# Kernel tuning notes

Hardware: AMD Instinct MI355X
Metric: run time of the kernel (lower is better)

The kernel has to match this reference:

```python
import jax, jax.numpy as jnp
import numpy as np

N, E, G = 50000, 300000, 64
VOCAB, EMB, FEAT = 10000, 64, 8
DIN, DH, EDIM = EMB * FEAT, 256, 6


def _lin(k, fout, fin):
    kw, kb = jax.random.split(k)
    w = jax.random.normal(kw, (fout, fin), jnp.float32) / float(np.sqrt(fin))
    b = jax.random.normal(kb, (fout,), jnp.float32) * 0.01
    return w, b


def setup_inputs() -> dict:
    key = jax.random.key(0)
    ks = jax.random.split(key, 10)
    inp = {
        'x_idx': jax.random.randint(ks[0], (N, FEAT), 0, VOCAB),
        'edge_index': jax.random.randint(ks[1], (2, E), 0, N),
        'edge_attr': jax.random.normal(ks[2], (E, EDIM), jnp.float32),
        'batch': jnp.sort(jax.random.randint(ks[3], (N,), 0, G)),
        'emb_table': jax.random.normal(ks[4], (VOCAB, EMB), jnp.float32) * 0.1,
    }
    # two TransformerConv layers: lin_query/key/value (d_in->DH), lin_edge (EDIM->DH), lin_skip (d_in->DH)
    for li, kbase, din in ((1, ks[5], DIN), (2, ks[6], DH)):
        sub = jax.random.split(kbase, 5)
        for j, (wn, bn, fin) in enumerate([('wq', 'bq', din), ('wk', 'bk', din), ('wv', 'bv', din), ('we', 'be', EDIM), ('ws', 'bs', din)]):
            w, b = _lin(sub[j], DH, fin)
            inp['c%d_%s' % (li, wn)] = w
            inp['c%d_%s' % (li, bn)] = b
    for i, (fout, fin, k) in enumerate([(256, 2 * DH, ks[7]), (128, 256, ks[8]), (1, 128, ks[9])]):
        w, b = _lin(k, fout, fin)
        inp['w%d' % (i + 1)] = w
        inp['b%d' % (i + 1)] = b
    return inp


def _tconv(h, src, dst, edge_attr, wq, bq, wk, bk, wv, bv, we, be, ws, bs):
    # PyG TransformerConv, heads=1, concat=True, root_weight=True, beta=False
    n = h.shape[0]
    q = h @ wq.T + bq                      # [N, DH]
    k = h @ wk.T + bk
    v = h @ wv.T + bv
    e = edge_attr @ we.T + be              # [E, DH]
    ke = k[src] + e                        # key fused with edge features
    logits = jnp.sum(q[dst] * ke, axis=-1) / jnp.sqrt(jnp.float32(DH))  # [E]
    m = jax.ops.segment_max(logits, dst, num_segments=n)
    m = jnp.where(jnp.isfinite(m), m, 0.0)
    a = jnp.exp(logits - m[dst])
    s = jax.ops.segment_sum(a, dst, num_segments=n)
    a = a / s[dst]                         # scatter-softmax over incoming edges
    agg = jax.ops.segment_sum((v[src] + e) * a[:, None], dst, num_segments=n)
    return agg + h @ ws.T + bs             # skip connection (root_weight)


def reference(x_idx, edge_index, edge_attr, batch, emb_table,
              c1_wq, c1_bq, c1_wk, c1_bk, c1_wv, c1_bv, c1_we, c1_be, c1_ws, c1_bs,
              c2_wq, c2_bq, c2_wk, c2_bk, c2_wv, c2_bv, c2_we, c2_be, c2_ws, c2_bs,
              w1, b1, w2, b2, w3, b3):
    x = emb_table[x_idx].reshape(x_idx.shape[0], DIN)  # [N, EMB*FEAT]
    src, dst = edge_index[0], edge_index[1]
    h = jax.nn.relu(_tconv(x, src, dst, edge_attr, c1_wq, c1_bq, c1_wk, c1_bk, c1_wv, c1_bv, c1_we, c1_be, c1_ws, c1_bs))
    h = jax.nn.relu(_tconv(h, src, dst, edge_attr, c2_wq, c2_bq, c2_wk, c2_bk, c2_wv, c2_bv, c2_we, c2_be, c2_ws, c2_bs))
    cnt = jax.ops.segment_sum(jnp.ones((h.shape[0],), h.dtype), batch, num_segments=G)
    gap = jax.ops.segment_sum(h, batch, num_segments=G) / jnp.maximum(cnt, 1.0)[:, None]
    gmp = jax.ops.segment_max(h, batch, num_segments=G)
    gmp = jnp.where(jnp.isfinite(gmp), gmp, 0.0)
    r = jnp.concatenate([gap, gmp], axis=1)             # [G, 2*DH]
    o = jax.nn.relu(r @ w1.T + b1)
    o = jax.nn.relu(o @ w2.T + b2)
    # dropout skipped (eval mode)
    return jax.nn.sigmoid(o @ w3.T + b3)[:, 0]          # [G]
```

## Files before the change

### kernel.cpp

```cpp
#include <hip/hip_runtime.h>

typedef unsigned long long ull;
typedef __bf16 bf16x8 __attribute__((ext_vector_type(8)));
typedef float f32x4 __attribute__((ext_vector_type(4)));

__device__ __forceinline__ float bf2f(unsigned short u) {
  union { unsigned int i; float f; } c; c.i = ((unsigned int)u) << 16; return c.f;
}
__device__ __forceinline__ unsigned short f2bf(float f) {
  union { float f; unsigned int i; } c; c.f = f;
  unsigned int u = c.i;
  u += 0x7fffu + ((u >> 16) & 1u);
  return (unsigned short)(u >> 16);
}

__global__ __launch_bounds__(256) void pack_weights(
    const float* __restrict__ wq, const float* __restrict__ wk,
    const float* __restrict__ wv, const float* __restrict__ ws,
    const float* __restrict__ bq, const float* __restrict__ bk,
    const float* __restrict__ bv, const float* __restrict__ bs,
    unsigned short* __restrict__ Wcat, float* __restrict__ bcat, int logK) {
  int idx = blockIdx.x * 256 + threadIdx.x;
  if (idx < 1024) {
    int rr = idx >> 8, cc = idx & 255;
    const float* bp = (rr == 0) ? bq : (rr == 1) ? bk : (rr == 2) ? bv : bs;
    bcat[idx] = bp[cc];
  }
  int K = 1 << logK;
  if (idx >= (1024 << logK)) return;
  int kj = idx & 7;
  int lane = (idx >> 3) & 63;
  int rg = (idx >> 9) & 3;
  int ksbits = logK - 5;
  int ks = (idx >> 11) & ((1 << ksbits) - 1);
  int colt = idx >> (11 + ksbits);
  int quad = lane >> 4, lm = lane & 15;
  int o = colt * 64 + rg * 16 + lm;
  int k = ks * 32 + quad * 8 + kj;
  int rr = o >> 8, oo = o & 255;
  const float* wp = (rr == 0) ? wq : (rr == 1) ? wk : (rr == 2) ? wv : ws;
  Wcat[idx] = f2bf(wp[oo * K + k]);
}

__global__ __launch_bounds__(256) void embed_gather(
    const int* __restrict__ x_idx, const float* __restrict__ emb,
    unsigned short* __restrict__ xbf, int total) {
  int idx = blockIdx.x * 256 + threadIdx.x;
  if (idx >= total) return;
  int n = idx >> 9, d = idx & 511, f = d >> 6, j = d & 63;
  int vi = x_idx[n * 8 + f];
  int n32 = n >> 5, lm = n & 15, half = (n >> 4) & 1;
  int ks = d >> 5, quad = (d >> 3) & 3, kj = d & 7;
  size_t a = (((size_t)(n32 * 16 + ks)) * 2 + half) * 512 + (quad * 16 + lm) * 8 + kj;
  xbf[a] = f2bf(emb[vi * 64 + j]);
}

__global__ __launch_bounds__(256) void count_dst(const int* __restrict__ dst,
                                                 int* __restrict__ counts, int E_) {
  int i = blockIdx.x * 256 + threadIdx.x;
  if (i < E_) atomicAdd(&counts[dst[i]], 1);
}

__global__ __launch_bounds__(256) void alloc_rows(const int* __restrict__ counts,
                                                  int* __restrict__ row_start,
                                                  int* __restrict__ cursor,
                                                  int* __restrict__ total, int n) {
  int i = blockIdx.x * 256 + threadIdx.x;
  int lane = threadIdx.x & 63;
  int c = (i < n) ? counts[i] : 0;
  int incl = c;
#pragma unroll
  for (int off = 1; off < 64; off <<= 1) {
    int t = __shfl_up(incl, off, 64);
    if (lane >= off) incl += t;
  }
  int base = 0;
  if (lane == 63) base = atomicAdd(total, incl);
  base = __shfl(base, 63, 64);
  int st = base + incl - c;
  if (i < n) { row_start[i] = st; cursor[i] = st; }
}

__global__ __launch_bounds__(256) void scatter_edges(
    const int* __restrict__ dst, const int* __restrict__ srcA,
    const float* __restrict__ eattr, int* __restrict__ cursor,
    int* __restrict__ srcs, float* __restrict__ ea_perm, int E_) {
  int i = blockIdx.x * 256 + threadIdx.x;
  if (i >= E_) return;
  int d = dst[i];
  int p = atomicAdd(&cursor[d], 1);
  srcs[p] = srcA[i];
  const float* ea = eattr + (size_t)i * 6;
  float* eo = ea_perm + (size_t)p * 6;
  eo[0] = ea[0]; eo[1] = ea[1]; eo[2] = ea[2];
  eo[3] = ea[3]; eo[4] = ea[4]; eo[5] = ea[5];
}

template <int K>
__global__ __launch_bounds__(256) void gemm_qkvs(
    const unsigned short* __restrict__ X, const unsigned short* __restrict__ W,
    const float* __restrict__ bcat,
    unsigned short* __restrict__ qout, unsigned short* __restrict__ kout,
    unsigned short* __restrict__ vout, float* __restrict__ sout,
    int Nn, int nrb) {
  __shared__ unsigned short Bs[2][4096];
  const int l = blockIdx.x;
  const int xcd = l & 7, j = l >> 3;
  const int q = nrb >> 3, r = nrb & 7;
  const int cnt = q + (xcd < r ? 1 : 0);
  const int lrb = j >> 4, colt = j & 15;
  if (lrb >= cnt) return;
  const int m_blk = xcd * q + min(xcd, r) + lrb;

  const int tid = threadIdx.x;
  const int wid = tid >> 6;
  const int lane = tid & 63;
  const int quad = lane >> 4, lm = lane & 15;
  const int m_base = m_blk * 128 + wid * 32;
  const int n_base = colt * 64;
  const size_t abase = (size_t)(m_blk * 4 + wid) * (K >> 5) * 1024 + lane * 8;
  const unsigned short* wchunk = W + (size_t)colt * (K >> 5) * 2048;
  const int nc = (K >> 5) >> 1;
  f32x4 acc[2][4] = {};

  {
    bf16x8 st0 = *(const bf16x8*)(wchunk + 0 * 2048 + tid * 8);
    bf16x8 st1 = *(const bf16x8*)(wchunk + 1 * 2048 + tid * 8);
    *(bf16x8*)(&Bs[0][0 * 2048 + tid * 8]) = st0;
    *(bf16x8*)(&Bs[0][1 * 2048 + tid * 8]) = st1;
  }
  __syncthreads();

  for (int c = 0; c < nc; c++) {
    bf16x8 st0, st1;
    const bool pf = (c + 1 < nc);
    if (pf) {
      const unsigned short* wp = wchunk + (size_t)(c + 1) * 4096;
      st0 = *(const bf16x8*)(wp + 0 * 2048 + tid * 8);
      st1 = *(const bf16x8*)(wp + 1 * 2048 + tid * 8);
    }
    const unsigned short* bs = &Bs[c & 1][0];
#pragma unroll
    for (int s = 0; s < 2; s++) {
      const int ks = c * 2 + s;
      const unsigned short* ap = X + abase + (size_t)ks * 1024;
      const unsigned short* bp = bs + s * 2048 + lane * 8;
      bf16x8 a0 = *(const bf16x8*)(ap);
      bf16x8 a1 = *(const bf16x8*)(ap + 512);
      bf16x8 b0 = *(const bf16x8*)(bp);
      bf16x8 b1 = *(const bf16x8*)(bp + 512);
      bf16x8 b2 = *(const bf16x8*)(bp + 1024);
      bf16x8 b3 = *(const bf16x8*)(bp + 1536);
      acc[0][0] = __builtin_amdgcn_mfma_f32_16x16x32_bf16(a0, b0, acc[0][0], 0, 0, 0);
      acc[0][1] = __builtin_amdgcn_mfma_f32_16x16x32_bf16(a0, b1, acc[0][1], 0, 0, 0);
      acc[0][2] = __builtin_amdgcn_mfma_f32_16x16x32_bf16(a0, b2, acc[0][2], 0, 0, 0);
      acc[0][3] = __builtin_amdgcn_mfma_f32_16x16x32_bf16(a0, b3, acc[0][3], 0, 0, 0);
      acc[1][0] = __builtin_amdgcn_mfma_f32_16x16x32_bf16(a1, b0, acc[1][0], 0, 0, 0);
      acc[1][1] = __builtin_amdgcn_mfma_f32_16x16x32_bf16(a1, b1, acc[1][1], 0, 0, 0);
      acc[1][2] = __builtin_amdgcn_mfma_f32_16x16x32_bf16(a1, b2, acc[1][2], 0, 0, 0);
      acc[1][3] = __builtin_amdgcn_mfma_f32_16x16x32_bf16(a1, b3, acc[1][3], 0, 0, 0);
    }
    if (pf) {
      unsigned short* bw = &Bs[(c + 1) & 1][0];
      *(bf16x8*)(bw + 0 * 2048 + tid * 8) = st0;
      *(bf16x8*)(bw + 1 * 2048 + tid * 8) = st1;
    }
    __syncthreads();
  }
#pragma unroll
  for (int mi = 0; mi < 2; mi++) {
#pragma unroll
    for (int r2 = 0; r2 < 4; r2++) {
      int row = m_base + mi * 16 + quad * 4 + r2;
      if (row >= Nn) continue;
      size_t rb = (size_t)row * 256;
#pragma unroll
      for (int ni = 0; ni < 4; ni++) {
        int col = n_base + ni * 16 + lm;
        float v = acc[mi][ni][r2] + bcat[col];
        int reg = col >> 8, c2 = col & 255;
        if (reg == 0)       qout[rb + c2] = f2bf(v * 0.0625f);
        else if (reg == 1)  kout[rb + c2] = f2bf(v);
        else if (reg == 2)  vout[rb + c2] = f2bf(v);
        else                sout[rb + c2] = v;
      }
    }
  }
}

__device__ __forceinline__ float dot4(ull uq, ull uk) {
  return bf2f((unsigned short)uq) * bf2f((unsigned short)uk)
       + bf2f((unsigned short)(uq >> 16)) * bf2f((unsigned short)(uk >> 16))
       + bf2f((unsigned short)(uq >> 32)) * bf2f((unsigned short)(uk >> 32))
       + bf2f((unsigned short)(uq >> 48)) * bf2f((unsigned short)(uk >> 48));
}

#define SEL8_F(a, t) ((t)==0?(a)[0]:(t)==1?(a)[1]:(t)==2?(a)[2]:(t)==3?(a)[3]:(t)==4?(a)[4]:(t)==5?(a)[5]:(t)==6?(a)[6]:(a)[7])

#define NPW 8
__global__ __launch_bounds__(256) void tconv_fused(
    const int* __restrict__ srcs, const int* __restrict__ row_start,
    const int* __restrict__ counts,
    const unsigned short* __restrict__ qv, const unsigned short* __restrict__ kv,
    const unsigned short* __restrict__ vv, const float* __restrict__ ea_perm,
    const float* __restrict__ skipv,
    const float* __restrict__ we, const float* __restrict__ be,
    int Nn, int mode,
    unsigned short* __restrict__ hout, float* __restrict__ h_acc) {
  __shared__ float we_s[1536];
  __shared__ float be_s[256];
  __shared__ float lgt[4][128];
  for (int i = threadIdx.x; i < 1536; i += 256) we_s[i] = we[i];
  be_s[threadIdx.x] = be[threadIdx.x];
  __syncthreads();
  int wid = threadIdx.x >> 6;
  int lane = threadIdx.x & 63;
  int wave = blockIdx.x * 4 + wid;
  int n0 = wave * NPW;
  if (n0 >= Nn) return;
  int n1 = min(n0 + NPW, Nn);
  int j0 = lane * 4;
  float* mylgt = lgt[wid];
  for (int n = n0; n < n1; n++) {
    int cnt = counts[n];
    float a0 = 0.f, a1 = 0.f, a2 = 0.f, a3 = 0.f;
    float e[4] = {0.f, 0.f, 0.f, 0.f};
    if (cnt > 0) {
      int beg = row_start[n];
      ull uqr = *(const ull*)(qv + (size_t)n * 256 + j0);
      float q0 = bf2f((unsigned short)uqr), q1 = bf2f((unsigned short)(uqr >> 16));
      float q2 = bf2f((unsigned short)(uqr >> 32)), q3 = bf2f((unsigned short)(uqr >> 48));
      float z[7];
#pragma unroll
      for (int t = 0; t < 6; t++) {
        z[t] = we_s[(j0 + 0) * 6 + t] * q0 + we_s[(j0 + 1) * 6 + t] * q1
             + we_s[(j0 + 2) * 6 + t] * q2 + we_s[(j0 + 3) * 6 + t] * q3;
      }
      z[6] = be_s[j0] * q0 + be_s[j0 + 1] * q1 + be_s[j0 + 2] * q2 + be_s[j0 + 3] * q3;
#pragma unroll
      for (int off = 32; off > 0; off >>= 1) {
#pragma unroll
        for (int t = 0; t < 7; t++) z[t] += __shfl_xor(z[t], off, 64);
      }
      for (int i0 = 0; i0 < cnt; i0 += 8) {
        int m = cnt - i0; if (m > 8) m = 8;
        int s8[8];
#pragma unroll
        for (int t = 0; t < 8; t++) {
          int pp = beg + i0 + ((t < m) ? t : (m - 1));
          s8[t] = srcs[pp];
        }
        ull uk[8];
#pragma unroll
        for (int t = 0; t < 8; t++)
          uk[t] = *(const ull*)(kv + (size_t)s8[t] * 256 + j0);
        float pv[8];
#pragma unroll
        for (int t = 0; t < 8; t++) pv[t] = dot4(uqr, uk[t]);
#pragma unroll
        for (int off = 32; off > 0; off >>= 1) {
#pragma unroll
          for (int t = 0; t < 8; t++) pv[t] += __shfl_xor(pv[t], off, 64);
        }
        if (lane < m) {
          int myp = beg + i0 + lane;
          const float* u = ea_perm + (size_t)myp * 6;
          float zd = z[0] * u[0] + z[1] * u[1] + z[2] * u[2]
                   + z[3] * u[3] + z[4] * u[4] + z[5] * u[5] + z[6];
          mylgt[i0 + lane] = SEL8_F(pv, lane) + zd;
        }
      }
      float lmx = -INFINITY;
      for (int b = lane; b < cnt; b += 64) lmx = fmaxf(lmx, mylgt[b]);
#pragma unroll
      for (int off = 32; off > 0; off >>= 1) lmx = fmaxf(lmx, __shfl_xor(lmx, off, 64));
      float se = 0.f;
      for (int b = lane; b < cnt; b += 64) se += __expf(mylgt[b] - lmx);
#pragma unroll
      for (int off = 32; off > 0; off >>= 1) se += __shfl_xor(se, off, 64);
      float inv = 1.f / se;
      float ub0 = 0.f, ub1 = 0.f, ub2 = 0.f, ub3 = 0.f, ub4 = 0.f, ub5 = 0.f;
      for (int i0 = 0; i0 < cnt; i0 += 8) {
        int m = cnt - i0; if (m > 8) m = 8;
        float wlane = 0.f;
        if (lane < m) {
          int myp = beg + i0 + lane;
          wlane = __expf(mylgt[i0 + lane] - lmx) * inv;
          const float* up = ea_perm + (size_t)myp * 6;
          ub0 += wlane * up[0]; ub1 += wlane * up[1]; ub2 += wlane * up[2];
          ub3 += wlane * up[3]; ub4 += wlane * up[4]; ub5 += wlane * up[5];
        }
        float w8[8];
        int s8[8];
#pragma unroll
        for (int t = 0; t < 8; t++) {
          w8[t] = __shfl(wlane, t, 64);
          int pp = beg + i0 + ((t < m) ? t : (m - 1));
          s8[t] = srcs[pp];
        }
        ull uv[8];
#pragma unroll
        for (int t = 0; t < 8; t++)
          uv[t] = *(const ull*)(vv + (size_t)s8[t] * 256 + j0);
#pragma unroll
        for (int t = 0; t < 8; t++) {
          float ww = w8[t];
          a0 += ww * bf2f((unsigned short)uv[t]);
          a1 += ww * bf2f((unsigned short)(uv[t] >> 16));
          a2 += ww * bf2f((unsigned short)(uv[t] >> 32));
          a3 += ww * bf2f((unsigned short)(uv[t] >> 48));
        }
      }
#pragma unroll
      for (int off = 1; off < 8; off <<= 1) {
        ub0 += __shfl_xor(ub0, off, 64); ub1 += __shfl_xor(ub1, off, 64);
        ub2 += __shfl_xor(ub2, off, 64); ub3 += __shfl_xor(ub3, off, 64);
        ub4 += __shfl_xor(ub4, off, 64); ub5 += __shfl_xor(ub5, off, 64);
      }
      ub0 = __shfl(ub0, 0, 64); ub1 = __shfl(ub1, 0, 64);
      ub2 = __shfl(ub2, 0, 64); ub3 = __shfl(ub3, 0, 64);
      ub4 = __shfl(ub4, 0, 64); ub5 = __shfl(ub5, 0, 64);
#pragma unroll
      for (int r = 0; r < 4; r++) {
        int d = j0 + r;
        e[r] = be_s[d]
             + we_s[d * 6 + 0] * ub0 + we_s[d * 6 + 1] * ub1 + we_s[d * 6 + 2] * ub2
             + we_s[d * 6 + 3] * ub3 + we_s[d * 6 + 4] * ub4 + we_s[d * 6 + 5] * ub5;
      }
    }
    float4 skv = *(const float4*)(skipv + (size_t)n * 256 + j0);
    float h0 = fmaxf(a0 + e[0] + skv.x, 0.f);
    float h1 = fmaxf(a1 + e[1] + skv.y, 0.f);
    float h2 = fmaxf(a2 + e[2] + skv.z, 0.f);
    float h3 = fmaxf(a3 + e[3] + skv.w, 0.f);
    if (mode == 0) {
      ull hv = (ull)f2bf(h0) | ((ull)f2bf(h1) << 16) | ((ull)f2bf(h2) << 32) | ((ull)f2bf(h3) << 48);
      int n32 = n >> 5, lmn = n & 15, halfn = (n >> 4) & 1;
      int ks = lane >> 3, quadc = (lane >> 1) & 3, kjc = (lane & 1) * 4;
      size_t a = (((size_t)(n32 * 8 + ks)) * 2 + halfn) * 512 + (quadc * 16 + lmn) * 8 + kjc;
      *(ull*)(hout + a) = hv;
    } else {
      float4 o; o.x = h0; o.y = h1; o.z = h2; o.w = h3;
      *(float4*)(h_acc + (size_t)n * 256 + j0) = o;
    }
  }
}

__global__ __launch_bounds__(256) void pool_reduce(
    const float* __restrict__ hfin, const int* __restrict__ batch, int Nn,
    float* __restrict__ gap, unsigned int* __restrict__ gmp) {
  int g = blockIdx.x, s = blockIdx.y, t = threadIdx.x;
  __shared__ int st_s, en_s;
  if (t == 0) {
    int lo = 0, hi = Nn;
    while (lo < hi) { int mid = (lo + hi) >> 1; if (batch[mid] < g) lo = mid + 1; else hi = mid; }
    st_s = lo;
    lo = 0; hi = Nn;
    while (lo < hi) { int mid = (lo + hi) >> 1; if (batch[mid] < g + 1) lo = mid + 1; else hi = mid; }
    en_s = lo;
  }
  __syncthreads();
  int st = st_s, en = en_s;
  int len = en - st;
  if (len <= 0) return;
  int nsplit = gridDim.y;
  int chunk = (len + nsplit - 1) / nsplit;
  int a = st + s * chunk;
  int b = min(a + chunk, en);
  if (a >= b) return;
  float acc = 0.f, mx = 0.f;
  for (int n = a; n < b; n++) {
    float v = hfin[(size_t)n * 256 + t];
    acc += v;
    mx = fmaxf(mx, v);
  }
  atomicAdd(&gap[(size_t)g * 256 + t], acc);
  atomicMax(&gmp[(size_t)g * 256 + t], __float_as_uint(mx));
}

__global__ __launch_bounds__(256) void pool_mlp(
    const float* __restrict__ gap, const unsigned int* __restrict__ gmp,
    const int* __restrict__ batch, int Nn,
    const float* __restrict__ w1, const float* __restrict__ b1,
    const float* __restrict__ w2, const float* __restrict__ b2,
    const float* __restrict__ w3, const float* __restrict__ b3,
    float* __restrict__ out) {
  int g = blockIdx.x, t = threadIdx.x;
  __shared__ float r[512];
  __shared__ float o1[256];
  __shared__ float o2[128];
  __shared__ float red[256];
  __shared__ int cnt_s;
  if (t == 0) {
    int lo = 0, hi = Nn;
    while (lo < hi) { int mid = (lo + hi) >> 1; if (batch[mid] < g) lo = mid + 1; else hi = mid; }
    int st = lo;
    lo = 0; hi = Nn;
    while (lo < hi) { int mid = (lo + hi) >> 1; if (batch[mid] < g + 1) lo = mid + 1; else hi = mid; }
    cnt_s = lo - st;
  }
  __syncthreads();
  float inv = 1.f / fmaxf((float)cnt_s, 1.f);
  r[t] = gap[(size_t)g * 256 + t] * inv;
  r[256 + t] = __uint_as_float(gmp[(size_t)g * 256 + t]);
  __syncthreads();
  {
    float a = b1[t];
    const float* wr = w1 + (size_t)t * 512;
    for (int k = 0; k < 512; k++) a += wr[k] * r[k];
    o1[t] = fmaxf(a, 0.f);
  }
  __syncthreads();
  if (t < 128) {
    float a = b2[t];
    const float* wr = w2 + (size_t)t * 256;
    for (int k = 0; k < 256; k++) a += wr[k] * o1[k];
    o2[t] = fmaxf(a, 0.f);
  }
  __syncthreads();
  red[t] = (t < 128) ? w3[t] * o2[t] : 0.f;
  __syncthreads();
  for (int s = 128; s > 0; s >>= 1) {
    if (t < s) red[t] += red[t + s];
    __syncthreads();
  }
  if (t == 0) out[g] = 1.f / (1.f + expf(-(red[0] + b3[0])));
}

extern "C" void kernel_launch(void* const* d_in, const int* in_sizes, int n_in,
                              void* d_out, int out_size, void* d_ws, size_t ws_size,
                              hipStream_t stream) {
  const int* x_idx      = (const int*)d_in[0];
  const int* edge_index = (const int*)d_in[1];
  const float* eattr    = (const float*)d_in[2];
  const int* batch      = (const int*)d_in[3];
  const float* emb      = (const float*)d_in[4];
  const float* c1_wq = (const float*)d_in[5],  *c1_bq = (const float*)d_in[6];
  const float* c1_wk = (const float*)d_in[7],  *c1_bk = (const float*)d_in[8];
  const float* c1_wv = (const float*)d_in[9],  *c1_bv = (const float*)d_in[10];
  const float* c1_we = (const float*)d_in[11], *c1_be = (const float*)d_in[12];
  const float* c1_ws = (const float*)d_in[13], *c1_bs = (const float*)d_in[14];
  const float* c2_wq = (const float*)d_in[15], *c2_bq = (const float*)d_in[16];
  const float* c2_wk = (const float*)d_in[17], *c2_bk = (const float*)d_in[18];
  const float* c2_wv = (const float*)d_in[19], *c2_bv = (const float*)d_in[20];
  const float* c2_we = (const float*)d_in[21], *c2_be = (const float*)d_in[22];
  const float* c2_ws = (const float*)d_in[23], *c2_bs = (const float*)d_in[24];
  const float* w1 = (const float*)d_in[25], *b1 = (const float*)d_in[26];
  const float* w2 = (const float*)d_in[27], *b2 = (const float*)d_in[28];
  const float* w3 = (const float*)d_in[29], *b3 = (const float*)d_in[30];

  const int Nn = in_sizes[3];
  const int Ee = in_sizes[1] / 2;
  const int nrb = (Nn + 127) / 128;

  char* ws = (char*)d_ws;
  size_t off = 0;
  auto alloc = [&](size_t bytes) -> void* {
    void* p = ws + off;
    off += (bytes + 255) & ~(size_t)255;
    return p;
  };
  unsigned short* xbf   = (unsigned short*)alloc((size_t)nrb * 128 * 512 * 2);
  unsigned short* qbf   = (unsigned short*)alloc((size_t)Nn * 256 * 2);
  unsigned short* kbf   = (unsigned short*)alloc((size_t)Nn * 256 * 2);
  unsigned short* vbf   = (unsigned short*)alloc((size_t)Nn * 256 * 2);
  float*          skipf = (float*)alloc((size_t)Nn * 256 * 4);
  unsigned short* h1bf  = (unsigned short*)alloc((size_t)nrb * 128 * 256 * 2);
  unsigned short* Wcat1 = (unsigned short*)alloc((size_t)1024 * 512 * 2);
  float*          bcat1 = (float*)alloc(1024 * 4);
  unsigned short* Wcat2 = (unsigned short*)alloc((size_t)1024 * 256 * 2);
  float*          bcat2 = (float*)alloc(1024 * 4);
  int*            counts    = (int*)alloc((size_t)Nn * 4);
  int*            row_start = (int*)alloc((size_t)Nn * 4);
  int*            cursor    = (int*)alloc((size_t)Nn * 4);
  int*            srcs      = (int*)alloc((size_t)Ee * 4);
  float*          ea_perm   = (float*)alloc((size_t)Ee * 6 * 4);
  int*            total     = (int*)alloc(256);
  float*          gap       = (float*)alloc((size_t)64 * 256 * 4);
  unsigned int*   gmp       = (unsigned int*)alloc((size_t)64 * 256 * 4);
  float* h_acc = (float*)xbf;

  const int* srcA = edge_index;
  const int* dstA = edge_index + Ee;

  hipMemsetAsync(counts, 0, (size_t)Nn * 4, stream);
  hipMemsetAsync(total, 0, 4, stream);
  hipMemsetAsync(gap, 0, (size_t)64 * 256 * 4, stream);
  hipMemsetAsync(gmp, 0, (size_t)64 * 256 * 4, stream);

  pack_weights<<<(1024 * 512 + 255) / 256, 256, 0, stream>>>(
      c1_wq, c1_wk, c1_wv, c1_ws, c1_bq, c1_bk, c1_bv, c1_bs, Wcat1, bcat1, 9);
  pack_weights<<<(1024 * 256 + 255) / 256, 256, 0, stream>>>(
      c2_wq, c2_wk, c2_wv, c2_ws, c2_bq, c2_bk, c2_bv, c2_bs, Wcat2, bcat2, 8);
  embed_gather<<<((Nn * 512) + 255) / 256, 256, 0, stream>>>(x_idx, emb, xbf, Nn * 512);
  count_dst<<<(Ee + 255) / 256, 256, 0, stream>>>(dstA, counts, Ee);
  alloc_rows<<<(Nn + 255) / 256, 256, 0, stream>>>(counts, row_start, cursor, total, Nn);
  scatter_edges<<<(Ee + 255) / 256, 256, 0, stream>>>(dstA, srcA, eattr, cursor,
                                                      srcs, ea_perm, Ee);

  const int rbmax = nrb / 8 + ((nrb % 8) ? 1 : 0);
  const int ggrid = 8 * rbmax * 16;
  const int sgrid = (Nn + NPW * 4 - 1) / (NPW * 4);

  gemm_qkvs<512><<<ggrid, 256, 0, stream>>>(xbf, Wcat1, bcat1, qbf, kbf, vbf,
                                            skipf, Nn, nrb);
  tconv_fused<<<sgrid, 256, 0, stream>>>(srcs, row_start, counts, qbf, kbf, vbf,
                                         ea_perm, skipf, c1_we, c1_be, Nn, 0,
                                         h1bf, nullptr);

  gemm_qkvs<256><<<ggrid, 256, 0, stream>>>(h1bf, Wcat2, bcat2, qbf, kbf, vbf,
                                            skipf, Nn, nrb);
  tconv_fused<<<sgrid, 256, 0, stream>>>(srcs, row_start, counts, qbf, kbf, vbf,
                                         ea_perm, skipf, c2_we, c2_be, Nn, 1,
                                         nullptr, h_acc);

  dim3 pg(64, 16);
  pool_reduce<<<pg, 256, 0, stream>>>(h_acc, batch, Nn, gap, gmp);
  pool_mlp<<<64, 256, 0, stream>>>(gap, gmp, batch, Nn, w1, b1, w2, b2, w3, b3,
                                   (float*)d_out);
}
```

Baseline: 709.4 us.

## Use online softmax to fuse logit and value aggregation into one edge pass

Replaces the three-pass scatter-softmax (compute logits into shared memory, reduce max/sum, then re-gather sources and V) with a single-pass online softmax. K and V rows for each 8-edge chunk are loaded together and the accumulators are rescaled by a running max. This removes the second read of srcs and the shared logit buffer, and lifts the old 128-edge cap on in-degree. It adds extra exp and rescale work per chunk, and nodes per wave are cut from 8 to 4 to spread work over more waves.

```diff
diff --git a/kernel.cpp b/kernel.cpp
--- a/kernel.cpp
+++ b/kernel.cpp
@@ -197,7 +197,7 @@
 
 #define SEL8_F(a, t) ((t)==0?(a)[0]:(t)==1?(a)[1]:(t)==2?(a)[2]:(t)==3?(a)[3]:(t)==4?(a)[4]:(t)==5?(a)[5]:(t)==6?(a)[6]:(a)[7])
 
-#define NPW 8
+#define NPW 4
 __global__ __launch_bounds__(256) void tconv_fused(
     const int* __restrict__ srcs, const int* __restrict__ row_start,
     const int* __restrict__ counts,
@@ -209,7 +209,6 @@
     unsigned short* __restrict__ hout, float* __restrict__ h_acc) {
   __shared__ float we_s[1536];
   __shared__ float be_s[256];
-  __shared__ float lgt[4][128];
   for (int i = threadIdx.x; i < 1536; i += 256) we_s[i] = we[i];
   be_s[threadIdx.x] = be[threadIdx.x];
   __syncthreads();
@@ -220,7 +219,6 @@
   if (n0 >= Nn) return;
   int n1 = min(n0 + NPW, Nn);
   int j0 = lane * 4;
-  float* mylgt = lgt[wid];
   for (int n = n0; n < n1; n++) {
     int cnt = counts[n];
     float a0 = 0.f, a1 = 0.f, a2 = 0.f, a3 = 0.f;
@@ -242,84 +240,80 @@
 #pragma unroll
         for (int t = 0; t < 7; t++) z[t] += __shfl_xor(z[t], off, 64);
       }
+      float mrun = -INFINITY, ssum = 0.f;
+      float ub0 = 0.f, ub1 = 0.f, ub2 = 0.f, ub3 = 0.f, ub4 = 0.f, ub5 = 0.f;
       for (int i0 = 0; i0 < cnt; i0 += 8) {
-        int m = cnt - i0; if (m > 8) m = 8;
+        int m8 = cnt - i0; if (m8 > 8) m8 = 8;
         int s8[8];
 #pragma unroll
         for (int t = 0; t < 8; t++) {
-          int pp = beg + i0 + ((t < m) ? t : (m - 1));
+          int pp = beg + i0 + ((t < m8) ? t : (m8 - 1));
           s8[t] = srcs[pp];
         }
-        ull uk[8];
+        ull uk8[8], uv8[8];
 #pragma unroll
         for (int t = 0; t < 8; t++)
-          uk[t] = *(const ull*)(kv + (size_t)s8[t] * 256 + j0);
+          uk8[t] = *(const ull*)(kv + (size_t)s8[t] * 256 + j0);
+#pragma unroll
+        for (int t = 0; t < 8; t++)
+          uv8[t] = *(const ull*)(vv + (size_t)s8[t] * 256 + j0);
         float pv[8];
 #pragma unroll
-        for (int t = 0; t < 8; t++) pv[t] = dot4(uqr, uk[t]);
+        for (int t = 0; t < 8; t++) pv[t] = dot4(uqr, uk8[t]);
 #pragma unroll
         for (int off = 32; off > 0; off >>= 1) {
 #pragma unroll
           for (int t = 0; t < 8; t++) pv[t] += __shfl_xor(pv[t], off, 64);
         }
-        if (lane < m) {
+        float zd = 0.f, uu0 = 0.f, uu1 = 0.f, uu2 = 0.f, uu3 = 0.f, uu4 = 0.f, uu5 = 0.f;
+        if (lane < m8) {
           int myp = beg + i0 + lane;
           const float* u = ea_perm + (size_t)myp * 6;
-          float zd = z[0] * u[0] + z[1] * u[1] + z[2] * u[2]
-                   + z[3] * u[3] + z[4] * u[4] + z[5] * u[5] + z[6];
-          mylgt[i0 + lane] = SEL8_F(pv, lane) + zd;
+          uu0 = u[0]; uu1 = u[1]; uu2 = u[2]; uu3 = u[3]; uu4 = u[4]; uu5 = u[5];
+          zd = z[0] * uu0 + z[1] * uu1 + z[2] * uu2
+             + z[3] * uu3 + z[4] * uu4 + z[5] * uu5 + z[6];
         }
-      }
-      float lmx = -INFINITY;
-      for (int b = lane; b < cnt; b += 64) lmx = fmaxf(lmx, mylgt[b]);
-#pragma unroll
-      for (int off = 32; off > 0; off >>= 1) lmx = fmaxf(lmx, __shfl_xor(lmx, off, 64));
-      float se = 0.f;
-      for (int b = lane; b < cnt; b += 64) se += __expf(mylgt[b] - lmx);
-#pragma unroll
-      for (int off = 32; off > 0; off >>= 1) se += __shfl_xor(se, off, 64);
-      float inv = 1.f / se;
-      float ub0 = 0.f, ub1 = 0.f, ub2 = 0.f, ub3 = 0.f, ub4 = 0.f, ub5 = 0.f;
-      for (int i0 = 0; i0 < cnt; i0 += 8) {
-        int m = cnt - i0; if (m > 8) m = 8;
-        float wlane = 0.f;
-        if (lane < m) {
-          int myp = beg + i0 + lane;
-          wlane = __expf(mylgt[i0 + lane] - lmx) * inv;
-          const float* up = ea_perm + (size_t)myp * 6;
-          ub0 += wlane * up[0]; ub1 += wlane * up[1]; ub2 += wlane * up[2];
-          ub3 += wlane * up[3]; ub4 += wlane * up[4]; ub5 += wlane * up[5];
-        }
+        float l8[8];
+#pragma unroll
+        for (int t = 0; t < 8; t++)
+          l8[t] = (t < m8) ? (pv[t] + __shfl(zd, t, 64)) : -INFINITY;
+        float bmax = l8[0];
+#pragma unroll
+        for (int t = 1; t < 8; t++) bmax = fmaxf(bmax, l8[t]);
+        float nm = fmaxf(mrun, bmax);
+        float sc = __expf(mrun - nm);
         float w8[8];
-        int s8[8];
-#pragma unroll
-        for (int t = 0; t < 8; t++) {
-          w8[t] = __shfl(wlane, t, 64);
-          int pp = beg + i0 + ((t < m) ? t : (m - 1));
-          s8[t] = srcs[pp];
-        }
-        ull uv[8];
-#pragma unroll
-        for (int t = 0; t < 8; t++)
-          uv[t] = *(const ull*)(vv + (size_t)s8[t] * 256 + j0);
+#pragma unroll
+        for (int t = 0; t < 8; t++) w8[t] = (t < m8) ? __expf(l8[t] - nm) : 0.f;
+        ssum = ssum * sc + ((w8[0] + w8[1]) + (w8[2] + w8[3]))
+                         + ((w8[4] + w8[5]) + (w8[6] + w8[7]));
+        a0 *= sc; a1 *= sc; a2 *= sc; a3 *= sc;
 #pragma unroll
         for (int t = 0; t < 8; t++) {
           float ww = w8[t];
-          a0 += ww * bf2f((unsigned short)uv[t]);
-          a1 += ww * bf2f((unsigned short)(uv[t] >> 16));
-          a2 += ww * bf2f((unsigned short)(uv[t] >> 32));
-          a3 += ww * bf2f((unsigned short)(uv[t] >> 48));
+          a0 += ww * bf2f((unsigned short)uv8[t]);
+          a1 += ww * bf2f((unsigned short)(uv8[t] >> 16));
+          a2 += ww * bf2f((unsigned short)(uv8[t] >> 32));
+          a3 += ww * bf2f((unsigned short)(uv8[t] >> 48));
         }
+        float wl = 0.f;
+        if (lane < m8) wl = __expf((SEL8_F(pv, lane) + zd) - nm);
+        ub0 = ub0 * sc + wl * uu0; ub1 = ub1 * sc + wl * uu1;
+        ub2 = ub2 * sc + wl * uu2; ub3 = ub3 * sc + wl * uu3;
+        ub4 = ub4 * sc + wl * uu4; ub5 = ub5 * sc + wl * uu5;
+        mrun = nm;
       }
+      float inv = 1.f / ssum;
+      a0 *= inv; a1 *= inv; a2 *= inv; a3 *= inv;
 #pragma unroll
       for (int off = 1; off < 8; off <<= 1) {
         ub0 += __shfl_xor(ub0, off, 64); ub1 += __shfl_xor(ub1, off, 64);
         ub2 += __shfl_xor(ub2, off, 64); ub3 += __shfl_xor(ub3, off, 64);
         ub4 += __shfl_xor(ub4, off, 64); ub5 += __shfl_xor(ub5, off, 64);
       }
-      ub0 = __shfl(ub0, 0, 64); ub1 = __shfl(ub1, 0, 64);
-      ub2 = __shfl(ub2, 0, 64); ub3 = __shfl(ub3, 0, 64);
-      ub4 = __shfl(ub4, 0, 64); ub5 = __shfl(ub5, 0, 64);
+      ub0 = __shfl(ub0, 0, 64) * inv; ub1 = __shfl(ub1, 0, 64) * inv;
+      ub2 = __shfl(ub2, 0, 64) * inv; ub3 = __shfl(ub3, 0, 64) * inv;
+      ub4 = __shfl(ub4, 0, 64) * inv; ub5 = __shfl(ub5, 0, 64) * inv;
 #pragma unroll
       for (int r = 0; r < 4; r++) {
         int d = j0 + r;
```

Result: no change. 699.4 us (-1.4%).
